# Optimization experiments

Hardware: AMD Instinct MI355X
Metric: run time of the kernel (lower is better)

The kernel has to match this reference:

```python
import jax, jax.numpy as jnp
import numpy as np

B, S, HIST = 2, 2048, 2048
H, HK, D = 16, 16, 128
DIM = H * D

def setup_inputs() -> dict:
    key = jax.random.key(0)
    ks = jax.random.split(key, 8)
    x = jax.random.normal(ks[0], (B, S, DIM), jnp.float32)
    prev_k = jax.random.normal(ks[1], (B, HIST, HK, D), jnp.float32)
    prev_v = jax.random.normal(ks[2], (B, HIST, HK, D), jnp.float32)
    # causal mask: history fully visible, causal within the current chunk
    q_pos = HIST + jnp.arange(S)
    k_pos = jnp.arange(HIST + S)
    mask = jnp.where(k_pos[None, :] <= q_pos[:, None], 0.0, -1e9).astype(jnp.float32)[None, None]
    sc = 0.02
    wq = jax.random.normal(ks[3], (DIM, DIM), jnp.float32) * sc
    wk = jax.random.normal(ks[4], (DIM, DIM), jnp.float32) * sc
    wv = jax.random.normal(ks[5], (DIM, DIM), jnp.float32) * sc
    wo = jax.random.normal(ks[6], (DIM, DIM), jnp.float32) * sc
    return {"x": x, "prev_k": prev_k, "prev_v": prev_v, "mask": mask,
            "wq": wq, "wk": wk, "wv": wv, "wo": wo}

def reference(x, prev_k, prev_v, mask, wq, wk, wv, wo):
    b, s, _ = x.shape
    # nn.Linear: y = x @ W^T, weights stored [out, in]
    xq = jnp.einsum('bsd,ed->bse', x, wq).reshape(b, s, H, D)
    xk = jnp.einsum('bsd,ed->bse', x, wk).reshape(b, s, HK, D)
    xv = jnp.einsum('bsd,ed->bse', x, wv).reshape(b, s, HK, D)
    k_all = jnp.concatenate([prev_k, xk], axis=1)  # [b, hist+s, hk, d]
    v_all = jnp.concatenate([prev_v, xv], axis=1)
    scores = jnp.einsum('bqhd,bkhd->bhqk', xq, k_all) / jnp.sqrt(jnp.float32(D))
    scores = scores + mask
    probs = jax.nn.softmax(scores.astype(jnp.float32), axis=-1).astype(xq.dtype)
    out = jnp.einsum('bhqk,bkhd->bqhd', probs, v_all).reshape(b, s, H * D)
    out = jnp.einsum('bse,de->bsd', out, wo)
    return out, k_all, v_all
```

## Files before the change

### kernel.cpp

```cpp
#include <hip/hip_runtime.h>
#include <math.h>

typedef __attribute__((ext_vector_type(8))) short bf16x8;
typedef __attribute__((ext_vector_type(4))) short bf16x4;
typedef __attribute__((ext_vector_type(4))) float f32x4;

#define SSCL (0.08838834764831845f * 1.4426950408889634f)

__device__ __forceinline__ short f2bf(float f) {
    union { float f; unsigned u; } x; x.f = f;
    unsigned r = x.u + 0x7fffu + ((x.u >> 16) & 1u);
    return (short)(r >> 16);
}
__device__ __forceinline__ float bf2f(short s) {
    union { unsigned u; float f; } x;
    x.u = ((unsigned)(unsigned short)s) << 16;
    return x.f;
}

typedef const __attribute__((address_space(1))) unsigned int* gas_ptr;
typedef __attribute__((address_space(3))) unsigned int* las_ptr;
__device__ __forceinline__ void async_copy16(const void* g, void* l) {
    __builtin_amdgcn_global_load_lds((gas_ptr)g, (las_ptr)l, 16, 0, 0);
}

__global__ __launch_bounds__(256)
void cvt_kernel(const float* __restrict__ src, short* __restrict__ dst, int n4) {
    int i = blockIdx.x * 256 + threadIdx.x;
    const int stride = gridDim.x * 256;
    for (; i < n4; i += stride) {
        float4 v = ((const float4*)src)[i];
        bf16x4 o;
        o[0] = f2bf(v.x); o[1] = f2bf(v.y); o[2] = f2bf(v.z); o[3] = f2bf(v.w);
        ((bf16x4*)dst)[i] = o;
    }
}

template<int QKV>
__global__ __launch_bounds__(256)
void gemm_kernel(const short* __restrict__ A,
                 const short* __restrict__ B0, const short* __restrict__ B1,
                 const short* __restrict__ B2,
                 short* __restrict__ D16, float* __restrict__ Dk,
                 float* __restrict__ Dv, float* __restrict__ Df) {
    __shared__ short As[128 * 64];
    __shared__ short Bs[128 * 64];
    const int tid = threadIdx.x, w = tid >> 6, ln = tid & 63;
    const int col = ln & 15, quad = ln >> 4;
    const int sel = QKV ? (blockIdx.x >> 4) : 0;
    const int tn = (blockIdx.x & 15) * 128;
    const int tm = blockIdx.y * 128;
    const short* B = (sel == 0) ? B0 : ((sel == 1) ? B1 : B2);

    const int wm = (w >> 1) * 64, wn = (w & 1) * 64;
    const int srow = ln >> 3, scol = (ln & 7) * 8;

    f32x4 acc[4][4];
    for (int i = 0; i < 4; ++i)
        for (int j = 0; j < 4; ++j)
            for (int e = 0; e < 4; ++e) acc[i][j][e] = 0.f;

    for (int k0 = 0; k0 < 2048; k0 += 64) {
        #pragma unroll
        for (int i = 0; i < 4; ++i) {
            int chunk = i * 4 + w;
            int row = chunk * 8 + srow;
            async_copy16(&A[(tm + row) * 2048 + k0 + scol], &As[chunk * 512]);
            async_copy16(&B[(tn + row) * 2048 + k0 + scol], &Bs[chunk * 512]);
        }
        asm volatile("s_waitcnt vmcnt(0)" ::: "memory");
        __syncthreads();
        #pragma unroll
        for (int kk = 0; kk < 2; ++kk) {
            bf16x8 af[4], bfr[4];
            #pragma unroll
            for (int i = 0; i < 4; ++i)
                af[i] = *(const bf16x8*)&As[(wm + i * 16 + col) * 64 + kk * 32 + quad * 8];
            #pragma unroll
            for (int j = 0; j < 4; ++j)
                bfr[j] = *(const bf16x8*)&Bs[(wn + j * 16 + col) * 64 + kk * 32 + quad * 8];
            __builtin_amdgcn_s_setprio(1);
            #pragma unroll
            for (int i = 0; i < 4; ++i)
                #pragma unroll
                for (int j = 0; j < 4; ++j)
                    acc[i][j] = __builtin_amdgcn_mfma_f32_16x16x32_bf16(af[i], bfr[j], acc[i][j], 0, 0, 0);
            __builtin_amdgcn_s_setprio(0);
        }
        __syncthreads();
    }
    for (int i = 0; i < 4; ++i)
        for (int j = 0; j < 4; ++j)
            for (int r = 0; r < 4; ++r) {
                int m = tm + wm + i * 16 + quad * 4 + r;
                int n = tn + wn + j * 16 + col;
                float v = acc[i][j][r];
                if (QKV) {
                    if (sel == 0) {
                        D16[m * 2048 + n] = f2bf(v);
                    } else {
                        int orow = m + ((m >> 11) + 1) * 2048;
                        float* D = (sel == 1) ? Dk : Dv;
                        D[orow * 2048 + n] = v;
                    }
                } else {
                    Df[m * 2048 + n] = v;
                }
            }
}

__global__ __launch_bounds__(256)
void prep_v(const float* __restrict__ Vall, short* __restrict__ Vtg) {
    __shared__ short L[64 * 132];
    const int tid = threadIdx.x;
    const int k0 = blockIdx.x * 64;
    const int h = blockIdx.y, b = blockIdx.z;
    const float* Vb = Vall + ((size_t)(b * 4096) * 16 + h) * 128;
    short* Vo = Vtg + ((size_t)(b * 16 + h) * 128) * 4096;
    #pragma unroll
    for (int i = 0; i < 8; ++i) {
        int idx = i * 256 + tid;
        int r = idx >> 5, c4 = (idx & 31) * 4;
        float4 v = *(const float4*)&Vb[(size_t)(k0 + r) * 2048 + c4];
        bf16x4 o4;
        o4[0] = f2bf(v.x); o4[1] = f2bf(v.y); o4[2] = f2bf(v.z); o4[3] = f2bf(v.w);
        *(bf16x4*)&L[r * 132 + c4] = o4;
    }
    __syncthreads();
    #pragma unroll
    for (int i = 0; i < 8; ++i) {
        int idx = i * 256 + tid;
        int d = idx >> 4, kc4 = (idx & 15) * 4;
        bf16x4 o4;
        o4[0] = L[(kc4 + 0) * 132 + d];
        o4[1] = L[(kc4 + 1) * 132 + d];
        o4[2] = L[(kc4 + 2) * 132 + d];
        o4[3] = L[(kc4 + 3) * 132 + d];
        *(bf16x4*)&Vo[(size_t)d * 4096 + k0 + (kc4 ^ ((d & 7) << 3))] = o4;
    }
}

__global__ __launch_bounds__(256)
void attn_mfma(const short* __restrict__ Q, const float* __restrict__ Kall,
               const short* __restrict__ Vtg, short* __restrict__ Ot) {
    __shared__ short Ks[2][64 * 128];
    __shared__ short Vs[2][128 * 64];
    __shared__ short Ps[4 * 16 * 72];
    const int tid = threadIdx.x, w = tid >> 6, ln = tid & 63;
    const int col = ln & 15, quad = ln >> 4;
    const int bh = blockIdx.x;
    const int b = bh >> 4, h = bh & 15;
    const int s0 = blockIdx.y * 64;
    const int xk = (col & 7) << 3;

    bf16x8 qf[4];
    {
        const int qr = (b * 2048 + s0 + w * 16 + col) * 2048 + h * 128;
        #pragma unroll
        for (int ks = 0; ks < 4; ++ks)
            qf[ks] = *(const bf16x8*)&Q[qr + ks * 32 + quad * 8];
    }
    f32x4 o[8];
    #pragma unroll
    for (int i = 0; i < 8; ++i)
        for (int e = 0; e < 4; ++e) o[i][e] = 0.f;
    float mr[4] = {-1e30f, -1e30f, -1e30f, -1e30f};
    float lr[4] = {0.f, 0.f, 0.f, 0.f};

    const float* Kb = Kall + ((size_t)(b * 4096) * 16 + h) * 128;
    const short* Vb = Vtg + ((size_t)(b * 16 + h) * 128) * 4096;
    short* PsW = &Ps[w * 1152];

    const int vd = (ln >> 3);
    const int vkofs = (ln & 7) * 8;
    const int kr0 = tid >> 5;
    const int kc4 = (tid & 31) * 4;
    const int kswz = (kc4 ^ ((kr0 & 7) << 3));

    const int ntiles = 33 + blockIdx.y;

    float4 kvr[8];

    #pragma unroll
    for (int i = 0; i < 8; ++i)
        kvr[i] = *(const float4*)&Kb[(size_t)(i * 8 + kr0) * 2048 + kc4];
    #pragma unroll
    for (int i = 0; i < 4; ++i) {
        int ch = i * 4 + w;
        async_copy16(&Vb[(size_t)(ch * 8 + vd) * 4096 + vkofs], &Vs[0][ch * 512]);
    }
    #pragma unroll
    for (int i = 0; i < 8; ++i) {
        bf16x4 kb4;
        kb4[0] = f2bf(kvr[i].x); kb4[1] = f2bf(kvr[i].y);
        kb4[2] = f2bf(kvr[i].z); kb4[3] = f2bf(kvr[i].w);
        *(bf16x4*)&Ks[0][(i * 8 + kr0) * 128 + kswz] = kb4;
    }
    asm volatile("s_waitcnt vmcnt(0)" ::: "memory");
    __syncthreads();

    for (int t = 0; t < ntiles; ++t) {
        const int p = t & 1;
        const int k0 = t * 64;
        const bool pf = (t + 1 < ntiles);

        if (pf) {
            const int k0n = k0 + 64;
            #pragma unroll
            for (int i = 0; i < 8; ++i)
                kvr[i] = *(const float4*)&Kb[(size_t)(k0n + i * 8 + kr0) * 2048 + kc4];
            #pragma unroll
            for (int i = 0; i < 4; ++i) {
                int ch = i * 4 + w;
                async_copy16(&Vb[(size_t)(ch * 8 + vd) * 4096 + k0n + vkofs],
                             &Vs[p ^ 1][ch * 512]);
            }
        }

        f32x4 s4[4];
        #pragma unroll
        for (int j = 0; j < 4; ++j)
            for (int e = 0; e < 4; ++e) s4[j][e] = 0.f;
        #pragma unroll
        for (int ks = 0; ks < 4; ++ks) {
            const int dofs = (ks * 32 + quad * 8) ^ xk;
            bf16x8 kf[4];
            #pragma unroll
            for (int j = 0; j < 4; ++j)
                kf[j] = *(const bf16x8*)&Ks[p][(j * 16 + col) * 128 + dofs];
            __builtin_amdgcn_s_setprio(1);
            #pragma unroll
            for (int j = 0; j < 4; ++j)
                s4[j] = __builtin_amdgcn_mfma_f32_16x16x32_bf16(qf[ks], kf[j], s4[j], 0, 0, 0);
            __builtin_amdgcn_s_setprio(0);
        }

        const bool full = (k0 + 63 <= 2048 + s0 + w * 16);
        float pp[4][4];
        if (full) {
            #pragma unroll
            for (int j = 0; j < 4; ++j)
                #pragma unroll
                for (int r = 0; r < 4; ++r) pp[j][r] = s4[j][r] * SSCL;
        } else {
            #pragma unroll
            for (int j = 0; j < 4; ++j) {
                int kp = k0 + j * 16 + col;
                #pragma unroll
                for (int r = 0; r < 4; ++r) {
                    int qp = 2048 + s0 + w * 16 + quad * 4 + r;
                    pp[j][r] = (kp <= qp) ? s4[j][r] * SSCL : -1e30f;
                }
            }
        }
        #pragma unroll
        for (int r = 0; r < 4; ++r) {
            float mx = fmaxf(fmaxf(pp[0][r], pp[1][r]), fmaxf(pp[2][r], pp[3][r]));
            mx = fmaxf(mx, __shfl_xor(mx, 1));
            mx = fmaxf(mx, __shfl_xor(mx, 2));
            mx = fmaxf(mx, __shfl_xor(mx, 4));
            mx = fmaxf(mx, __shfl_xor(mx, 8));
            float mn = fmaxf(mr[r], mx);
            float al = exp2f(mr[r] - mn);
            mr[r] = mn;
            float rs = 0.f;
            #pragma unroll
            for (int j = 0; j < 4; ++j) { pp[j][r] = exp2f(pp[j][r] - mn); rs += pp[j][r]; }
            rs += __shfl_xor(rs, 1);
            rs += __shfl_xor(rs, 2);
            rs += __shfl_xor(rs, 4);
            rs += __shfl_xor(rs, 8);
            lr[r] = lr[r] * al + rs;
            #pragma unroll
            for (int i = 0; i < 8; ++i) o[i][r] *= al;
        }
        #pragma unroll
        for (int j = 0; j < 4; ++j)
            #pragma unroll
            for (int r = 0; r < 4; ++r)
                PsW[(quad * 4 + r) * 72 + j * 16 + col] = f2bf(pp[j][r]);
        bf16x8 pa0 = *(const bf16x8*)&PsW[col * 72 + quad * 8];
        bf16x8 pa1 = *(const bf16x8*)&PsW[col * 72 + 32 + quad * 8];
        #pragma unroll
        for (int dt = 0; dt < 8; ++dt) {
            int row = dt * 16 + col;
            bf16x8 v0 = *(const bf16x8*)&Vs[p][row * 64 + ((quad * 8) ^ xk)];
            bf16x8 v1 = *(const bf16x8*)&Vs[p][row * 64 + ((32 + quad * 8) ^ xk)];
            __builtin_amdgcn_s_setprio(1);
            o[dt] = __builtin_amdgcn_mfma_f32_16x16x32_bf16(pa0, v0, o[dt], 0, 0, 0);
            o[dt] = __builtin_amdgcn_mfma_f32_16x16x32_bf16(pa1, v1, o[dt], 0, 0, 0);
            __builtin_amdgcn_s_setprio(0);
        }

        if (pf) {
            #pragma unroll
            for (int i = 0; i < 8; ++i) {
                bf16x4 kb4;
                kb4[0] = f2bf(kvr[i].x); kb4[1] = f2bf(kvr[i].y);
                kb4[2] = f2bf(kvr[i].z); kb4[3] = f2bf(kvr[i].w);
                *(bf16x4*)&Ks[p ^ 1][(i * 8 + kr0) * 128 + kswz] = kb4;
            }
        }
        asm volatile("s_waitcnt vmcnt(0)" ::: "memory");
        __syncthreads();
    }
    const int orow = (b * 2048 + s0 + w * 16) * 2048 + h * 128;
    #pragma unroll
    for (int r = 0; r < 4; ++r) {
        float inv = 1.f / lr[r];
        #pragma unroll
        for (int dt = 0; dt < 8; ++dt)
            Ot[orow + (quad * 4 + r) * 2048 + dt * 16 + col] = f2bf(o[dt][r] * inv);
    }
}

extern "C" void kernel_launch(void* const* d_in, const int* in_sizes, int n_in,
                              void* d_out, int out_size, void* d_ws, size_t ws_size,
                              hipStream_t stream) {
    const float* x  = (const float*)d_in[0];
    const float* pk = (const float*)d_in[1];
    const float* pv = (const float*)d_in[2];
    const float* wq = (const float*)d_in[4];
    const float* wk = (const float*)d_in[5];
    const float* wv = (const float*)d_in[6];
    const float* wo = (const float*)d_in[7];

    float* out  = (float*)d_out;
    float* kall = out + 8388608;
    float* vall = out + 25165824;

    short* ws16 = (short*)d_ws;
    short* xb  = ws16;
    short* wqb = ws16 + 8388608;
    short* wkb = ws16 + 12582912;
    short* wvb = ws16 + 16777216;
    short* wob = ws16 + 20971520;
    short* vtg = ws16 + 8388608;
    short* qbf = ws16 + 25165824;
    short* ot  = xb;

    hipMemcpyAsync(kall,           pk,           16777216u, hipMemcpyDeviceToDevice, stream);
    hipMemcpyAsync(kall + 8388608, pk + 4194304, 16777216u, hipMemcpyDeviceToDevice, stream);
    hipMemcpyAsync(vall,           pv,           16777216u, hipMemcpyDeviceToDevice, stream);
    hipMemcpyAsync(vall + 8388608, pv + 4194304, 16777216u, hipMemcpyDeviceToDevice, stream);

    cvt_kernel<<<1024, 256, 0, stream>>>(x,  xb,  2097152);
    cvt_kernel<<<512,  256, 0, stream>>>(wq, wqb, 1048576);
    cvt_kernel<<<512,  256, 0, stream>>>(wk, wkb, 1048576);
    cvt_kernel<<<512,  256, 0, stream>>>(wv, wvb, 1048576);

    gemm_kernel<1><<<dim3(48, 32), 256, 0, stream>>>(xb, wqb, wkb, wvb,
                                                     qbf, kall, vall, nullptr);
    prep_v<<<dim3(64, 16, 2), 256, 0, stream>>>(vall, vtg);
    attn_mfma<<<dim3(32, 32), 256, 0, stream>>>(qbf, kall, vtg, ot);
    cvt_kernel<<<512, 256, 0, stream>>>(wo, wob, 1048576);
    gemm_kernel<0><<<dim3(16, 32), 256, 0, stream>>>(ot, wob, wob, wob,
                                                     nullptr, nullptr, nullptr, out);
}
```

Baseline: 858.3 us.

## Pre-convert K to swizzled bf16 and async-load it into LDS in attention

After: 834.8 us. -2.7%, faster.

```diff
diff --git a/kernel.cpp b/kernel.cpp
--- a/kernel.cpp
+++ b/kernel.cpp
@@ -26,6 +26,22 @@
 
 __global__ __launch_bounds__(256)
 void cvt_kernel(const float* __restrict__ src, short* __restrict__ dst, int n4) {
+    int i = blockIdx.x * 256 + threadIdx.x;
+    const int stride = gridDim.x * 256;
+    for (; i < n4; i += stride) {
+        float4 v = ((const float4*)src)[i];
+        bf16x4 o;
+        o[0] = f2bf(v.x); o[1] = f2bf(v.y); o[2] = f2bf(v.z); o[3] = f2bf(v.w);
+        ((bf16x4*)dst)[i] = o;
+    }
+}
+
+__global__ __launch_bounds__(256)
+void cvt3_kernel(const float* __restrict__ s0, const float* __restrict__ s1,
+                 const float* __restrict__ s2, short* __restrict__ d0,
+                 short* __restrict__ d1, short* __restrict__ d2, int n4) {
+    const float* src = (blockIdx.y == 0) ? s0 : ((blockIdx.y == 1) ? s1 : s2);
+    short* dst = (blockIdx.y == 0) ? d0 : ((blockIdx.y == 1) ? d1 : d2);
     int i = blockIdx.x * 256 + threadIdx.x;
     const int stride = gridDim.x * 256;
     for (; i < n4; i += stride) {
@@ -110,13 +126,25 @@
 }
 
 __global__ __launch_bounds__(256)
-void prep_v(const float* __restrict__ Vall, short* __restrict__ Vtg) {
+void prep_kv(const float* __restrict__ Kall, const float* __restrict__ Vall,
+             short* __restrict__ Ktg, short* __restrict__ Vtg) {
     __shared__ short L[64 * 132];
     const int tid = threadIdx.x;
     const int k0 = blockIdx.x * 64;
     const int h = blockIdx.y, b = blockIdx.z;
+    const float* Kb = Kall + ((size_t)(b * 4096) * 16 + h) * 128;
     const float* Vb = Vall + ((size_t)(b * 4096) * 16 + h) * 128;
+    short* Ko = Ktg + ((size_t)(b * 16 + h) * 4096) * 128;
     short* Vo = Vtg + ((size_t)(b * 16 + h) * 128) * 4096;
+    #pragma unroll
+    for (int i = 0; i < 8; ++i) {
+        int idx = i * 256 + tid;
+        int kr = idx >> 5, c4 = (idx & 31) * 4;
+        float4 v = *(const float4*)&Kb[(size_t)(k0 + kr) * 2048 + c4];
+        bf16x4 o4;
+        o4[0] = f2bf(v.x); o4[1] = f2bf(v.y); o4[2] = f2bf(v.z); o4[3] = f2bf(v.w);
+        *(bf16x4*)&Ko[(size_t)(k0 + kr) * 128 + (c4 ^ ((kr & 7) << 3))] = o4;
+    }
     #pragma unroll
     for (int i = 0; i < 8; ++i) {
         int idx = i * 256 + tid;
@@ -141,7 +169,7 @@
 }
 
 __global__ __launch_bounds__(256)
-void attn_mfma(const short* __restrict__ Q, const float* __restrict__ Kall,
+void attn_mfma(const short* __restrict__ Q, const short* __restrict__ Ktg,
                const short* __restrict__ Vtg, short* __restrict__ Ot) {
     __shared__ short Ks[2][64 * 128];
     __shared__ short Vs[2][128 * 64];
@@ -167,34 +195,22 @@
     float mr[4] = {-1e30f, -1e30f, -1e30f, -1e30f};
     float lr[4] = {0.f, 0.f, 0.f, 0.f};
 
-    const float* Kb = Kall + ((size_t)(b * 4096) * 16 + h) * 128;
+    const short* Kb = Ktg + ((size_t)(b * 16 + h) * 4096) * 128;
     const short* Vb = Vtg + ((size_t)(b * 16 + h) * 128) * 4096;
     short* PsW = &Ps[w * 1152];
 
+    const int kr4 = ln >> 4;
+    const int kc8 = (ln & 15) * 8;
     const int vd = (ln >> 3);
     const int vkofs = (ln & 7) * 8;
-    const int kr0 = tid >> 5;
-    const int kc4 = (tid & 31) * 4;
-    const int kswz = (kc4 ^ ((kr0 & 7) << 3));
 
     const int ntiles = 33 + blockIdx.y;
 
-    float4 kvr[8];
-
-    #pragma unroll
-    for (int i = 0; i < 8; ++i)
-        kvr[i] = *(const float4*)&Kb[(size_t)(i * 8 + kr0) * 2048 + kc4];
     #pragma unroll
     for (int i = 0; i < 4; ++i) {
         int ch = i * 4 + w;
+        async_copy16(&Kb[(size_t)(ch * 4 + kr4) * 128 + kc8], &Ks[0][ch * 512]);
         async_copy16(&Vb[(size_t)(ch * 8 + vd) * 4096 + vkofs], &Vs[0][ch * 512]);
-    }
-    #pragma unroll
-    for (int i = 0; i < 8; ++i) {
-        bf16x4 kb4;
-        kb4[0] = f2bf(kvr[i].x); kb4[1] = f2bf(kvr[i].y);
-        kb4[2] = f2bf(kvr[i].z); kb4[3] = f2bf(kvr[i].w);
-        *(bf16x4*)&Ks[0][(i * 8 + kr0) * 128 + kswz] = kb4;
     }
     asm volatile("s_waitcnt vmcnt(0)" ::: "memory");
     __syncthreads();
@@ -207,11 +223,10 @@
         if (pf) {
             const int k0n = k0 + 64;
             #pragma unroll
-            for (int i = 0; i < 8; ++i)
-                kvr[i] = *(const float4*)&Kb[(size_t)(k0n + i * 8 + kr0) * 2048 + kc4];
-            #pragma unroll
             for (int i = 0; i < 4; ++i) {
                 int ch = i * 4 + w;
+                async_copy16(&Kb[(size_t)(k0n + ch * 4 + kr4) * 128 + kc8],
+                             &Ks[p ^ 1][ch * 512]);
                 async_copy16(&Vb[(size_t)(ch * 8 + vd) * 4096 + k0n + vkofs],
                              &Vs[p ^ 1][ch * 512]);
             }
@@ -292,15 +307,6 @@
             __builtin_amdgcn_s_setprio(0);
         }
 
-        if (pf) {
-            #pragma unroll
-            for (int i = 0; i < 8; ++i) {
-                bf16x4 kb4;
-                kb4[0] = f2bf(kvr[i].x); kb4[1] = f2bf(kvr[i].y);
-                kb4[2] = f2bf(kvr[i].z); kb4[3] = f2bf(kvr[i].w);
-                *(bf16x4*)&Ks[p ^ 1][(i * 8 + kr0) * 128 + kswz] = kb4;
-            }
-        }
         asm volatile("s_waitcnt vmcnt(0)" ::: "memory");
         __syncthreads();
     }
@@ -338,21 +344,20 @@
     short* vtg = ws16 + 8388608;
     short* qbf = ws16 + 25165824;
     short* ot  = xb;
+    short* ktg = (short*)out;
 
     hipMemcpyAsync(kall,           pk,           16777216u, hipMemcpyDeviceToDevice, stream);
     hipMemcpyAsync(kall + 8388608, pk + 4194304, 16777216u, hipMemcpyDeviceToDevice, stream);
     hipMemcpyAsync(vall,           pv,           16777216u, hipMemcpyDeviceToDevice, stream);
     hipMemcpyAsync(vall + 8388608, pv + 4194304, 16777216u, hipMemcpyDeviceToDevice, stream);
 
-    cvt_kernel<<<1024, 256, 0, stream>>>(x,  xb,  2097152);
-    cvt_kernel<<<512,  256, 0, stream>>>(wq, wqb, 1048576);
-    cvt_kernel<<<512,  256, 0, stream>>>(wk, wkb, 1048576);
-    cvt_kernel<<<512,  256, 0, stream>>>(wv, wvb, 1048576);
+    cvt_kernel<<<1024, 256, 0, stream>>>(x, xb, 2097152);
+    cvt3_kernel<<<dim3(512, 3), 256, 0, stream>>>(wq, wk, wv, wqb, wkb, wvb, 1048576);
 
     gemm_kernel<1><<<dim3(48, 32), 256, 0, stream>>>(xb, wqb, wkb, wvb,
                                                      qbf, kall, vall, nullptr);
-    prep_v<<<dim3(64, 16, 2), 256, 0, stream>>>(vall, vtg);
-    attn_mfma<<<dim3(32, 32), 256, 0, stream>>>(qbf, kall, vtg, ot);
+    prep_kv<<<dim3(64, 16, 2), 256, 0, stream>>>(kall, vall, ktg, vtg);
+    attn_mfma<<<dim3(32, 32), 256, 0, stream>>>(qbf, ktg, vtg, ot);
     cvt_kernel<<<512, 256, 0, stream>>>(wo, wob, 1048576);
     gemm_kernel<0><<<dim3(16, 32), 256, 0, stream>>>(ot, wob, wob, wob,
                                                      nullptr, nullptr, nullptr, out);
```
